# Kernel optimization log

Measured on AMD Instinct MI355X. Metric: run time of the kernel, lower is better.

The kernel has to match this reference:

```python
import jax, jax.numpy as jnp
import numpy as np

N_NODES = 50000
N_EDGES = 800000
D = 128
L = 3


def setup_inputs() -> dict:
    key = jax.random.key(0)
    k1, k2, k3 = jax.random.split(key, 3)
    x = jax.random.normal(k1, (N_NODES, D), dtype=jnp.float32)
    edge_index = jax.random.randint(k2, (2, N_EDGES), 0, N_NODES, dtype=jnp.int64)
    # per-layer GCNConv weights [L, in, out], bias [L, out] (zeros, as nn.Linear default bias is small),
    # PReLU per-channel slopes initialized to 0.25 (torch default)
    Ws = jax.random.normal(k3, (L, D, D), dtype=jnp.float32) / np.sqrt(D)
    bs = jnp.zeros((L, D), dtype=jnp.float32)
    alphas = jnp.full((L, D), 0.25, dtype=jnp.float32)
    return {"x": x, "edge_index": edge_index, "Ws": Ws, "bs": bs, "alphas": alphas}


def reference(x, edge_index, Ws, bs, alphas):
    N = x.shape[0]
    # PyG gcn_norm with edge_weight=None: unit weights, add self-loops (fill value 1),
    # symmetric normalization deg^{-1/2}[row] * deg^{-1/2}[col], aggregate at col (target).
    loop = jnp.arange(N, dtype=edge_index.dtype)
    row = jnp.concatenate([edge_index[0], loop])  # [E+N] source
    col = jnp.concatenate([edge_index[1], loop])  # [E+N] target
    deg = jax.ops.segment_sum(jnp.ones(row.shape[0], x.dtype), col, num_segments=N)
    dinv = jax.lax.rsqrt(deg)  # deg >= 1 due to self-loops
    norm = dinv[row] * dinv[col]  # [E+N]

    z = x
    for l in range(Ws.shape[0]):
        h = z @ Ws[l]  # linear transform [N, D]
        # gather -> scale -> scatter-add aggregation
        agg = jax.ops.segment_sum(h[row] * norm[:, None], col, num_segments=N)
        out = agg + bs[l]
        z = jnp.where(out >= 0, out, alphas[l] * out)  # per-channel PReLU
    return z
```

## Files before the change

### kernel.cpp

```cpp
#include <hip/hip_runtime.h>

#define N_NODES 50000
#define N_EDGES 800000
#define D 128
#define L 3
#define SCAN_B 1024
#define SCAN_NB ((N_NODES + SCAN_B - 1) / SCAN_B)


__global__ __launch_bounds__(256) void deg_init_k(unsigned int* deg) {
  int i = blockIdx.x * 256 + threadIdx.x;
  if (i < N_NODES) deg[i] = 1u;
}

__global__ __launch_bounds__(256) void deg_count_k(const int* __restrict__ col,
                                                   unsigned int* deg,
                                                   unsigned int* __restrict__ rank) {
  int e = blockIdx.x * 256 + threadIdx.x;
  if (e < N_EDGES) rank[e] = atomicAdd(&deg[col[e]], 1u);
}

__global__ __launch_bounds__(256) void dinv_k(float* dinv_f, const unsigned int* deg) {
  int i = blockIdx.x * 256 + threadIdx.x;
  if (i < N_NODES) dinv_f[i] = rsqrtf((float)deg[i]);
}

__global__ __launch_bounds__(SCAN_B) void scan1_k(const unsigned int* __restrict__ deg,
                                                  unsigned int* __restrict__ rowptr,
                                                  unsigned int* __restrict__ bsum) {
  __shared__ unsigned int buf[SCAN_B];
  const int tid = threadIdx.x;
  const int i = blockIdx.x * SCAN_B + tid;
  unsigned int d = (i < N_NODES) ? (deg[i] - 1u) : 0u;
  buf[tid] = d;
  __syncthreads();
  for (int off = 1; off < SCAN_B; off <<= 1) {
    unsigned int t = (tid >= off) ? buf[tid - off] : 0u;
    __syncthreads();
    buf[tid] += t;
    __syncthreads();
  }
  if (i < N_NODES) rowptr[i] = buf[tid] - d;
  if (tid == SCAN_B - 1) bsum[blockIdx.x] = buf[tid];
}

__global__ __launch_bounds__(64) void scan2_k(const unsigned int* __restrict__ bsum,
                                              unsigned int* __restrict__ boff,
                                              unsigned int* __restrict__ rowptr) {
  int lane = threadIdx.x;
  unsigned int v = (lane < SCAN_NB) ? bsum[lane] : 0u;
  unsigned int incl = v;
#pragma unroll
  for (int off = 1; off < 64; off <<= 1) {
    unsigned int t = __shfl_up(incl, off, 64);
    if (lane >= off) incl += t;
  }
  if (lane < SCAN_NB) boff[lane] = incl - v;
  if (lane == 63) rowptr[N_NODES] = incl;
}

__global__ __launch_bounds__(SCAN_B) void scan3_k(const unsigned int* __restrict__ boff,
                                                  unsigned int* __restrict__ rowptr) {
  int i = blockIdx.x * SCAN_B + threadIdx.x;
  if (i < N_NODES) rowptr[i] += boff[blockIdx.x];
}

__global__ __launch_bounds__(256) void fill_k(const int* __restrict__ rows,
                                              const int* __restrict__ cols,
                                              const unsigned int* __restrict__ rowptr,
                                              const unsigned int* __restrict__ rank,
                                              unsigned int* __restrict__ csr) {
  int e = blockIdx.x * 256 + threadIdx.x;
  if (e >= N_EDGES) return;
  csr[rowptr[cols[e]] + rank[e] - 1u] = (unsigned int)rows[e];
}

__global__ __launch_bounds__(256) void gather_k(const unsigned int* __restrict__ rowptr,
                                                const unsigned int* __restrict__ csr,
                                                const float* __restrict__ dinv,
                                                const float* __restrict__ Z,
                                                float* __restrict__ AGG) {
  int wid = (blockIdx.x * 256 + threadIdx.x) >> 6;
  int lane = threadIdx.x & 63;
  if (wid >= N_NODES) return;
  const float2* Z2 = (const float2*)Z;
  float di = dinv[wid];
  float2 z = Z2[(size_t)wid * 64 + lane];
  float sx = di * z.x, sy = di * z.y;
  unsigned int p0 = rowptr[wid], p1 = rowptr[wid + 1];
  for (unsigned int base = p0; base < p1; base += 64u) {
    unsigned int cnt = p1 - base;
    if (cnt > 64u) cnt = 64u;
    unsigned int s = 0u;
    float w = 0.f;
    if (lane < (int)cnt) {
      s = csr[base + lane];
      w = dinv[s];
    }
    unsigned int j = 0;
    for (; j + 8u <= cnt; j += 8u) {
      unsigned int ss[8];
      float wws[8];
#pragma unroll
      for (int t = 0; t < 8; ++t) {
        ss[t] = __shfl(s, (int)(j + t), 64);
        wws[t] = __shfl(w, (int)(j + t), 64);
      }
      float2 v[8];
#pragma unroll
      for (int t = 0; t < 8; ++t) v[t] = Z2[(size_t)ss[t] * 64 + lane];
#pragma unroll
      for (int t = 0; t < 8; ++t) {
        sx += wws[t] * v[t].x;
        sy += wws[t] * v[t].y;
      }
    }
    for (; j < cnt; ++j) {
      unsigned int s0 = __shfl(s, (int)j, 64);
      float w0 = __shfl(w, (int)j, 64);
      float2 v0 = Z2[(size_t)s0 * 64 + lane];
      sx += w0 * v0.x;
      sy += w0 * v0.y;
    }
  }
  float2 r;
  r.x = sx * di;
  r.y = sy * di;
  ((float2*)AGG)[(size_t)wid * 64 + lane] = r;
}

__global__ __launch_bounds__(256) void gemm_k(const float* __restrict__ P,
                                              const float* __restrict__ W,
                                              const float* __restrict__ bias,
                                              const float* __restrict__ alpha,
                                              float* __restrict__ out) {
  __shared__ float sW[32 * 128];
  __shared__ float sZT[32 * 132];
  const int tid = threadIdx.x;
  const int rb = blockIdx.x * 128;
  const int rg = tid >> 4, cg = tid & 15;
  const int r0 = rg * 8, c0 = cg * 8;
  float acc[8][8];
#pragma unroll
  for (int i = 0; i < 8; ++i)
#pragma unroll
    for (int j = 0; j < 8; ++j) acc[i][j] = 0.f;

  for (int kc = 0; kc < 128; kc += 32) {
    const float4* Wg = (const float4*)(W + (size_t)kc * 128);
#pragma unroll
    for (int i = 0; i < 4; ++i)
      ((float4*)sW)[tid + i * 256] = Wg[tid + i * 256];
#pragma unroll
    for (int i = 0; i < 4; ++i) {
      int idx = tid + i * 256;
      int r = idx >> 3, k4 = idx & 7;
      int gr = rb + r;
      float4 v = make_float4(0.f, 0.f, 0.f, 0.f);
      if (gr < N_NODES) v = *(const float4*)(P + (size_t)gr * D + kc + k4 * 4);
      sZT[(k4 * 4 + 0) * 132 + r] = v.x;
      sZT[(k4 * 4 + 1) * 132 + r] = v.y;
      sZT[(k4 * 4 + 2) * 132 + r] = v.z;
      sZT[(k4 * 4 + 3) * 132 + r] = v.w;
    }
    __syncthreads();
#pragma unroll 8
    for (int k = 0; k < 32; ++k) {
      float4 za = *(const float4*)&sZT[k * 132 + r0];
      float4 zb = *(const float4*)&sZT[k * 132 + r0 + 4];
      float4 wa = *(const float4*)&sW[k * 128 + c0];
      float4 wb = *(const float4*)&sW[k * 128 + c0 + 4];
      float zz[8] = {za.x, za.y, za.z, za.w, zb.x, zb.y, zb.z, zb.w};
      float ww[8] = {wa.x, wa.y, wa.z, wa.w, wb.x, wb.y, wb.z, wb.w};
#pragma unroll
      for (int i = 0; i < 8; ++i)
#pragma unroll
        for (int j = 0; j < 8; ++j) acc[i][j] = fmaf(zz[i], ww[j], acc[i][j]);
    }
    __syncthreads();
  }

  float bl[8], al[8];
#pragma unroll
  for (int j = 0; j < 8; ++j) {
    bl[j] = bias[c0 + j];
    al[j] = alpha[c0 + j];
  }
#pragma unroll
  for (int i = 0; i < 8; ++i) {
    int gr = rb + r0 + i;
    if (gr >= N_NODES) continue;
    float o[8];
#pragma unroll
    for (int j = 0; j < 8; ++j) {
      float v = acc[i][j] + bl[j];
      o[j] = v >= 0.f ? v : al[j] * v;
    }
    float4* dst = (float4*)(out + (size_t)gr * D + c0);
    dst[0] = make_float4(o[0], o[1], o[2], o[3]);
    dst[1] = make_float4(o[4], o[5], o[6], o[7]);
  }
}


extern "C" void kernel_launch(void* const* d_in, const int* in_sizes, int n_in,
                              void* d_out, int out_size, void* d_ws, size_t ws_size,
                              hipStream_t stream) {
  const float* x      = (const float*)d_in[0];
  const int*   ei     = (const int*)d_in[1];
  const float* Ws     = (const float*)d_in[2];
  const float* bs     = (const float*)d_in[3];
  const float* alphas = (const float*)d_in[4];
  float* out = (float*)d_out;

  const int* rows = ei;
  const int* cols = ei + N_EDGES;

  char* ws = (char*)d_ws;
  const size_t NPAD = (((size_t)N_NODES * 4 + 255) / 256) * 256;
  const size_t NP1PAD = ((((size_t)N_NODES + 1) * 4 + 255) / 256) * 256;
  float*        dinv   = (float*)ws;             ws += NPAD;
  unsigned int* rowptr = (unsigned int*)ws;      ws += NP1PAD;
  unsigned int* deg    = (unsigned int*)ws;      ws += NPAD;
  unsigned int* bsum   = (unsigned int*)ws;      ws += 256;
  unsigned int* boff   = (unsigned int*)ws;      ws += 256;
  unsigned int* csr    = (unsigned int*)ws;      ws += (size_t)N_EDGES * 4;
  float*        AGG    = (float*)ws;
  unsigned int* rank = (unsigned int*)AGG;
  float* Z = out;

  deg_init_k<<<(N_NODES + 255) / 256, 256, 0, stream>>>(deg);
  deg_count_k<<<(N_EDGES + 255) / 256, 256, 0, stream>>>(cols, deg, rank);
  dinv_k<<<(N_NODES + 255) / 256, 256, 0, stream>>>(dinv, deg);
  scan1_k<<<SCAN_NB, SCAN_B, 0, stream>>>(deg, rowptr, bsum);
  scan2_k<<<1, 64, 0, stream>>>(bsum, boff, rowptr);
  scan3_k<<<SCAN_NB, SCAN_B, 0, stream>>>(boff, rowptr);
  fill_k<<<(N_EDGES + 255) / 256, 256, 0, stream>>>(rows, cols, rowptr, rank, csr);

  for (int l = 0; l < L; ++l) {
    const float* zin = (l == 0) ? x : Z;
    gather_k<<<(N_NODES * 64 + 255) / 256, 256, 0, stream>>>(rowptr, csr, dinv, zin, AGG);
    gemm_k<<<(N_NODES + 127) / 128, 256, 0, stream>>>(
        AGG, Ws + (size_t)l * D * D, bs + (size_t)l * D, alphas + (size_t)l * D, Z);
  }
}
```

Before: 338.2 us.

## Replace FP32 SIMT GEMM with split-bf16 MFMA GEMM

```diff
diff --git a/kernel.cpp b/kernel.cpp
--- a/kernel.cpp
+++ b/kernel.cpp
@@ -6,6 +6,14 @@
 #define L 3
 #define SCAN_B 1024
 #define SCAN_NB ((N_NODES + SCAN_B - 1) / SCAN_B)
+
+typedef __attribute__((ext_vector_type(8))) short short8;
+typedef __attribute__((ext_vector_type(16))) float f32x16;
+
+__device__ __forceinline__ unsigned int bf16_rne(float f) {
+  unsigned int u = __float_as_uint(f);
+  return (u + 0x7FFFu + ((u >> 16) & 1u)) >> 16;
+}
 
 
 __global__ __launch_bounds__(256) void deg_init_k(unsigned int* deg) {
@@ -129,76 +137,85 @@
   ((float2*)AGG)[(size_t)wid * 64 + lane] = r;
 }
 
-__global__ __launch_bounds__(256) void gemm_k(const float* __restrict__ P,
-                                              const float* __restrict__ W,
-                                              const float* __restrict__ bias,
-                                              const float* __restrict__ alpha,
-                                              float* __restrict__ out) {
-  __shared__ float sW[32 * 128];
-  __shared__ float sZT[32 * 132];
+__global__ __launch_bounds__(256) void gemm_mfma_k(const float* __restrict__ P,
+                                                   const float* __restrict__ W,
+                                                   const float* __restrict__ bias,
+                                                   const float* __restrict__ alpha,
+                                                   float* __restrict__ out) {
+  __shared__ unsigned int sWhi[128 * 36];
+  __shared__ unsigned int sWlo[128 * 36];
   const int tid = threadIdx.x;
+  const int lane = tid & 63;
+  const int w = tid >> 6;
+  const int kg = lane >> 5;
+  const int cl = lane & 31;
   const int rb = blockIdx.x * 128;
-  const int rg = tid >> 4, cg = tid & 15;
-  const int r0 = rg * 8, c0 = cg * 8;
-  float acc[8][8];
-#pragma unroll
-  for (int i = 0; i < 8; ++i)
-#pragma unroll
-    for (int j = 0; j < 8; ++j) acc[i][j] = 0.f;
-
-  for (int kc = 0; kc < 128; kc += 32) {
-    const float4* Wg = (const float4*)(W + (size_t)kc * 128);
-#pragma unroll
-    for (int i = 0; i < 4; ++i)
-      ((float4*)sW)[tid + i * 256] = Wg[tid + i * 256];
-#pragma unroll
-    for (int i = 0; i < 4; ++i) {
-      int idx = tid + i * 256;
-      int r = idx >> 3, k4 = idx & 7;
-      int gr = rb + r;
-      float4 v = make_float4(0.f, 0.f, 0.f, 0.f);
-      if (gr < N_NODES) v = *(const float4*)(P + (size_t)gr * D + kc + k4 * 4);
-      sZT[(k4 * 4 + 0) * 132 + r] = v.x;
-      sZT[(k4 * 4 + 1) * 132 + r] = v.y;
-      sZT[(k4 * 4 + 2) * 132 + r] = v.z;
-      sZT[(k4 * 4 + 3) * 132 + r] = v.w;
+  const int row = rb + w * 32 + cl;
+  const int ar = row < N_NODES ? row : N_NODES - 1;
+
+  f32x16 acc[4];
+#pragma unroll
+  for (int cf = 0; cf < 4; ++cf)
+#pragma unroll
+    for (int j = 0; j < 16; ++j) acc[cf][j] = 0.f;
+
+  for (int h = 0; h < 2; ++h) {
+    const int k0 = h * 64;
+    if (h) __syncthreads();
+#pragma unroll
+    for (int j = 0; j < 16; ++j) {
+      int id = j * 256 + tid;
+      int c = id & 127;
+      int kd = id >> 7;
+      float w0 = W[(size_t)(k0 + kd * 2) * 128 + c];
+      float w1 = W[(size_t)(k0 + kd * 2 + 1) * 128 + c];
+      unsigned int h0 = bf16_rne(w0), h1 = bf16_rne(w1);
+      float f0 = __uint_as_float(h0 << 16), f1 = __uint_as_float(h1 << 16);
+      unsigned int l0 = bf16_rne(w0 - f0), l1 = bf16_rne(w1 - f1);
+      sWhi[c * 36 + kd] = h0 | (h1 << 16);
+      sWlo[c * 36 + kd] = l0 | (l1 << 16);
     }
     __syncthreads();
-#pragma unroll 8
-    for (int k = 0; k < 32; ++k) {
-      float4 za = *(const float4*)&sZT[k * 132 + r0];
-      float4 zb = *(const float4*)&sZT[k * 132 + r0 + 4];
-      float4 wa = *(const float4*)&sW[k * 128 + c0];
-      float4 wb = *(const float4*)&sW[k * 128 + c0 + 4];
-      float zz[8] = {za.x, za.y, za.z, za.w, zb.x, zb.y, zb.z, zb.w};
-      float ww[8] = {wa.x, wa.y, wa.z, wa.w, wb.x, wb.y, wb.z, wb.w};
-#pragma unroll
-      for (int i = 0; i < 8; ++i)
-#pragma unroll
-        for (int j = 0; j < 8; ++j) acc[i][j] = fmaf(zz[i], ww[j], acc[i][j]);
-    }
-    __syncthreads();
-  }
-
-  float bl[8], al[8];
-#pragma unroll
-  for (int j = 0; j < 8; ++j) {
-    bl[j] = bias[c0 + j];
-    al[j] = alpha[c0 + j];
-  }
-#pragma unroll
-  for (int i = 0; i < 8; ++i) {
-    int gr = rb + r0 + i;
-    if (gr >= N_NODES) continue;
-    float o[8];
-#pragma unroll
-    for (int j = 0; j < 8; ++j) {
-      float v = acc[i][j] + bl[j];
-      o[j] = v >= 0.f ? v : al[j] * v;
-    }
-    float4* dst = (float4*)(out + (size_t)gr * D + c0);
-    dst[0] = make_float4(o[0], o[1], o[2], o[3]);
-    dst[1] = make_float4(o[4], o[5], o[6], o[7]);
+
+#pragma unroll
+    for (int ks4 = 0; ks4 < 4; ++ks4) {
+      const float4* ap = (const float4*)(P + (size_t)ar * D + k0 + ks4 * 16 + kg * 8);
+      float4 a0 = ap[0], a1 = ap[1];
+      float af[8] = {a0.x, a0.y, a0.z, a0.w, a1.x, a1.y, a1.z, a1.w};
+      short8 ahi, alo;
+#pragma unroll
+      for (int i = 0; i < 8; ++i) {
+        unsigned int hb = bf16_rne(af[i]);
+        float hf = __uint_as_float(hb << 16);
+        unsigned int lb = bf16_rne(af[i] - hf);
+        ahi[i] = (short)hb;
+        alo[i] = (short)lb;
+      }
+#pragma unroll
+      for (int cf = 0; cf < 4; ++cf) {
+        int cc = cf * 32 + cl;
+        int off = cc * 36 + ks4 * 8 + kg * 4;
+        short8 bhi = *(const short8*)&sWhi[off];
+        short8 blo = *(const short8*)&sWlo[off];
+        acc[cf] = __builtin_amdgcn_mfma_f32_32x32x16_bf16(ahi, bhi, acc[cf], 0, 0, 0);
+        acc[cf] = __builtin_amdgcn_mfma_f32_32x32x16_bf16(ahi, blo, acc[cf], 0, 0, 0);
+        acc[cf] = __builtin_amdgcn_mfma_f32_32x32x16_bf16(alo, bhi, acc[cf], 0, 0, 0);
+      }
+    }
+  }
+
+#pragma unroll
+  for (int cf = 0; cf < 4; ++cf) {
+    int col = cf * 32 + cl;
+    float bl = bias[col], al = alpha[col];
+#pragma unroll
+    for (int j = 0; j < 16; ++j) {
+      int r = rb + w * 32 + 4 * kg + (j & 3) + 8 * (j >> 2);
+      if (r < N_NODES) {
+        float v = acc[cf][j] + bl;
+        out[(size_t)r * D + col] = v >= 0.f ? v : al * v;
+      }
+    }
   }
 }
 
@@ -224,7 +241,7 @@
   unsigned int* deg    = (unsigned int*)ws;      ws += NPAD;
   unsigned int* bsum   = (unsigned int*)ws;      ws += 256;
   unsigned int* boff   = (unsigned int*)ws;      ws += 256;
-  unsigned int* csr    = (unsigned int*)ws;      ws += (size_t)N_EDGES * 4;
+  unsigned int* csr    = (unsigned int*)ws;      ws += (((size_t)N_EDGES + 16) * 4 + 255) / 256 * 256;
   float*        AGG    = (float*)ws;
   unsigned int* rank = (unsigned int*)AGG;
   float* Z = out;
@@ -240,7 +257,7 @@
   for (int l = 0; l < L; ++l) {
     const float* zin = (l == 0) ? x : Z;
     gather_k<<<(N_NODES * 64 + 255) / 256, 256, 0, stream>>>(rowptr, csr, dinv, zin, AGG);
-    gemm_k<<<(N_NODES + 127) / 128, 256, 0, stream>>>(
+    gemm_mfma_k<<<(N_NODES + 127) / 128, 256, 0, stream>>>(
         AGG, Ws + (size_t)l * D * D, bs + (size_t)l * D, alphas + (size_t)l * D, Z);
   }
 }
```

New measurement: 304.0 us. -10.1%, faster.
